# Performance work log

Measured on AMD Instinct MI355X. Metric: run time of the kernel, lower is better.

## Reference

```python
import jax, jax.numpy as jnp
import numpy as np

EMB_LEN = 1024
HEAD_SIZE = 64

def setup_inputs() -> dict:
    key = jax.random.key(0)
    k1, k2, k3, k4 = jax.random.split(key, 4)
    input_emb = jax.random.normal(k1, (8, 4096, EMB_LEN), dtype=jnp.float32)
    # nn.Linear weights are [out, in]; applied as x @ W.T
    Wq = jax.random.normal(k2, (HEAD_SIZE, EMB_LEN), dtype=jnp.float32) * (EMB_LEN ** -0.5)
    Wk = jax.random.normal(k3, (HEAD_SIZE, EMB_LEN), dtype=jnp.float32) * (EMB_LEN ** -0.5)
    Wv = jax.random.normal(k4, (HEAD_SIZE, EMB_LEN), dtype=jnp.float32) * (EMB_LEN ** -0.5)
    return {"input_emb": input_emb, "Wq": Wq, "Wk": Wk, "Wv": Wv}

def reference(input_emb, Wq, Wk, Wv):
    B, S, E = input_emb.shape
    scale = jnp.asarray(HEAD_SIZE, input_emb.dtype) ** -0.5
    q = jnp.einsum('bse,he->bsh', input_emb, Wq)  # [B,S,H]
    k = jnp.einsum('bse,he->bsh', input_emb, Wk)
    v = jnp.einsum('bse,he->bsh', input_emb, Wv)
    scores = jnp.einsum('bqh,bkh->bqk', q, k) * scale  # [B,S,S]
    causal = jnp.tril(jnp.ones((S, S), dtype=bool))
    scores = jnp.where(causal, scores, -jnp.inf)
    attn = jax.nn.softmax(scores, axis=-1)
    return jnp.einsum('bqk,bkh->bqh', attn, v)
```

## Files before the change

### kernel.cpp

```cpp
#include <hip/hip_runtime.h>
#include <hip/hip_bf16.h>

#define EMB 1024
#define HS 64
#define SEQ 4096

using bf16x8 = __attribute__((ext_vector_type(8))) __bf16;
using f32x4  = __attribute__((ext_vector_type(4))) float;

__device__ __forceinline__ ushort f2b(float f) {
    unsigned x = __float_as_uint(f);
    return (ushort)((x + 0x7fffu + ((x >> 16) & 1u)) >> 16);
}

__global__ void cvt_w(const float* __restrict__ wq, const float* __restrict__ wk,
                      const float* __restrict__ wv, ushort* __restrict__ wcat) {
    int i = blockIdx.x * 256 + threadIdx.x;
    const int n = HS * EMB;
    if (i >= 3 * n) return;
    float f;
    if (i < n)          f = wq[i];
    else if (i < 2 * n) f = wk[i - n];
    else                f = wv[i - 2 * n];
    wcat[i] = f2b(f);
}

__global__ __launch_bounds__(1024) void qkv_proj(
        const float* __restrict__ x, const ushort* __restrict__ wcat,
        ushort* __restrict__ qo, ushort* __restrict__ ko, ushort* __restrict__ vo) {
    __shared__ ushort Xs[64][72];
    __shared__ ushort Ws[192][72];
    const int t = threadIdx.x;
    const int lane = t & 63, wid = t >> 6;
    const int g = lane >> 4, c = lane & 15;
    const int strip = wid >> 2, colq = wid & 3;
    const int row0 = blockIdx.x * 64;

    f32x4 acc[3];
#pragma unroll
    for (int i = 0; i < 3; ++i) acc[i] = f32x4{0.f, 0.f, 0.f, 0.f};

    for (int kc = 0; kc < EMB; kc += 64) {
        __syncthreads();
        {
            int e = t * 4, r = e >> 6, cc = e & 63;
            float4 v = *reinterpret_cast<const float4*>(&x[(row0 + r) * EMB + kc + cc]);
            ushort4 u;
            u.x = f2b(v.x); u.y = f2b(v.y); u.z = f2b(v.z); u.w = f2b(v.w);
            *reinterpret_cast<ushort4*>(&Xs[r][cc]) = u;
        }
#pragma unroll
        for (int i = 0; i < 3; ++i) {
            int e = (i * 1024 + t) * 4, r = e >> 6, cc = e & 63;
            *reinterpret_cast<ushort4*>(&Ws[r][cc]) =
                *reinterpret_cast<const ushort4*>(&wcat[r * EMB + kc + cc]);
        }
        __syncthreads();
#pragma unroll
        for (int kk = 0; kk < 2; ++kk) {
            bf16x8 a = *reinterpret_cast<const bf16x8*>(&Xs[strip * 16 + c][kk * 32 + 8 * g]);
#pragma unroll
            for (int nt = 0; nt < 3; ++nt) {
                bf16x8 b = *reinterpret_cast<const bf16x8*>(
                    &Ws[(colq * 3 + nt) * 16 + c][kk * 32 + 8 * g]);
                acc[nt] = __builtin_amdgcn_mfma_f32_16x16x32_bf16(a, b, acc[nt], 0, 0, 0);
            }
        }
    }

    const float qs = 0.125f * 1.44269504f;
#pragma unroll
    for (int nt = 0; nt < 3; ++nt) {
        int col = (colq * 3 + nt) * 16 + c;
        int rowb = row0 + strip * 16 + 4 * g;
        if (col < 64) {
#pragma unroll
            for (int r = 0; r < 4; ++r)
                qo[(rowb + r) * 64 + col] = f2b(acc[nt][r] * qs);
        } else if (col < 128) {
#pragma unroll
            for (int r = 0; r < 4; ++r)
                ko[(rowb + r) * 64 + (col - 64)] = f2b(acc[nt][r]);
        } else {
            int b = rowb >> 12, s0 = rowb & 4095;
            ushort4 pv;
            pv.x = f2b(acc[nt][0]); pv.y = f2b(acc[nt][1]);
            pv.z = f2b(acc[nt][2]); pv.w = f2b(acc[nt][3]);
            *reinterpret_cast<ushort4*>(&vo[(b * 64 + (col - 128)) * SEQ + s0]) = pv;
        }
    }
}

__global__ __launch_bounds__(256) void attn(
        const ushort* __restrict__ q, const ushort* __restrict__ k,
        const ushort* __restrict__ vt, float* __restrict__ out) {
    __shared__ __align__(16) char smem[33280];

    const int t = threadIdx.x;
    const int lane = t & 63, w = t >> 6;
    const int g = lane >> 4, c = lane & 15;

    const int bid = blockIdx.x;
    const int batch = bid & 7;
    const int qt = 127 - (bid >> 3);
    const int q0 = qt * 32;
    const int nch = qt + 1;
    const int c0 = (w * nch) >> 2, c1 = ((w + 1) * nch) >> 2;

    const ushort* qb = q  + (size_t)batch * SEQ * 64;
    const ushort* kb = k  + (size_t)batch * SEQ * 64;
    const ushort* vb = vt + (size_t)batch * 64 * SEQ;

    bf16x8 qa[2][2];
#pragma unroll
    for (int ss = 0; ss < 2; ++ss)
#pragma unroll
        for (int kk = 0; kk < 2; ++kk)
            qa[ss][kk] = *reinterpret_cast<const bf16x8*>(
                &qb[(q0 + ss * 16 + c) * 64 + kk * 32 + 8 * g]);

    f32x4 accO[2][4];
#pragma unroll
    for (int ss = 0; ss < 2; ++ss)
#pragma unroll
        for (int nt = 0; nt < 4; ++nt) accO[ss][nt] = f32x4{0.f, 0.f, 0.f, 0.f};
    float lsum[2][4] = {{0.f, 0.f, 0.f, 0.f}, {0.f, 0.f, 0.f, 0.f}};

    char* const pslice = smem + w * 2048;
    const int pwr = (c >> 3) * 256 + g * 64 + (c & 7) * 2;

    auto loadkv = [&](bf16x8 (&kf)[2][2], bf16x8 (&vf)[4], int ch) {
        const int kv0 = ch * 32;
#pragma unroll
        for (int kt = 0; kt < 2; ++kt)
#pragma unroll
            for (int kk = 0; kk < 2; ++kk)
                kf[kt][kk] = *reinterpret_cast<const bf16x8*>(
                    &kb[(kv0 + kt * 16 + c) * 64 + kk * 32 + 8 * g]);
#pragma unroll
        for (int nt = 0; nt < 4; ++nt)
            vf[nt] = *reinterpret_cast<const bf16x8*>(
                &vb[(nt * 16 + c) * SEQ + kv0 + 8 * g]);
    };

    auto compute = [&](bf16x8 (&kf)[2][2], bf16x8 (&vf)[4], int ch) {
        f32x4 sA[2][2];
#pragma unroll
        for (int ss = 0; ss < 2; ++ss)
#pragma unroll
            for (int kt = 0; kt < 2; ++kt) sA[ss][kt] = f32x4{0.f, 0.f, 0.f, 0.f};
        __builtin_amdgcn_s_setprio(1);
#pragma unroll
        for (int kk = 0; kk < 2; ++kk)
#pragma unroll
            for (int kt = 0; kt < 2; ++kt) {
                sA[0][kt] = __builtin_amdgcn_mfma_f32_16x16x32_bf16(qa[0][kk], kf[kt][kk], sA[0][kt], 0, 0, 0);
                sA[1][kt] = __builtin_amdgcn_mfma_f32_16x16x32_bf16(qa[1][kk], kf[kt][kk], sA[1][kt], 0, 0, 0);
            }
        __builtin_amdgcn_s_setprio(0);

        if (ch == nch - 1) {
#pragma unroll
            for (int ss = 0; ss < 2; ++ss)
#pragma unroll
                for (int kt = 0; kt < 2; ++kt)
#pragma unroll
                    for (int r = 0; r < 4; ++r)
                        if (kt * 16 + c > ss * 16 + 4 * g + r) sA[ss][kt][r] = -INFINITY;
        }

#pragma unroll
        for (int ss = 0; ss < 2; ++ss)
#pragma unroll
            for (int kt = 0; kt < 2; ++kt)
#pragma unroll
                for (int r = 0; r < 4; ++r) {
                    float p = __builtin_amdgcn_exp2f(sA[ss][kt][r]);
                    lsum[ss][r] += p;
                    *(ushort*)(pslice + ss * 1024 + kt * 512 + r * 16 + pwr) = f2b(p);
                }

        bf16x8 pa0 = *reinterpret_cast<const bf16x8*>(pslice + lane * 16);
        bf16x8 pa1 = *reinterpret_cast<const bf16x8*>(pslice + 1024 + lane * 16);

        __builtin_amdgcn_s_setprio(1);
#pragma unroll
        for (int nt = 0; nt < 4; ++nt) {
            accO[0][nt] = __builtin_amdgcn_mfma_f32_16x16x32_bf16(pa0, vf[nt], accO[0][nt], 0, 0, 0);
            accO[1][nt] = __builtin_amdgcn_mfma_f32_16x16x32_bf16(pa1, vf[nt], accO[1][nt], 0, 0, 0);
        }
        __builtin_amdgcn_s_setprio(0);
    };

    bf16x8 kfA[2][2], vfA[4], kfB[2][2], vfB[4];
    int ch = c0;
    if (ch < c1) {
        loadkv(kfA, vfA, ch);
        while (true) {
            loadkv(kfB, vfB, (ch + 1 < c1) ? ch + 1 : ch);
            compute(kfA, vfA, ch);
            if (++ch >= c1) break;
            loadkv(kfA, vfA, (ch + 1 < c1) ? ch + 1 : ch);
            compute(kfB, vfB, ch);
            if (++ch >= c1) break;
        }
    }

#pragma unroll
    for (int off = 1; off < 16; off <<= 1)
#pragma unroll
        for (int ss = 0; ss < 2; ++ss)
#pragma unroll
            for (int r = 0; r < 4; ++r)
                lsum[ss][r] += __shfl_xor(lsum[ss][r], off, 64);

    __syncthreads();
#pragma unroll
    for (int ss = 0; ss < 2; ++ss)
#pragma unroll
        for (int nt = 0; nt < 4; ++nt)
#pragma unroll
            for (int r = 0; r < 4; ++r)
                *(float*)(smem + w * 8192 + (ss * 16 + 4 * g + r) * 256 + (nt * 16 + c) * 4) =
                    accO[ss][nt][r];
    if (c == 0) {
#pragma unroll
        for (int ss = 0; ss < 2; ++ss)
#pragma unroll
            for (int r = 0; r < 4; ++r)
                *(float*)(smem + 32768 + w * 128 + (ss * 16 + 4 * g + r) * 4) = lsum[ss][r];
    }
    __syncthreads();

    float* ob = out + (size_t)batch * SEQ * 64;
    const int col = t & 63, r0 = t >> 6;
#pragma unroll
    for (int rr = 0; rr < 8; ++rr) {
        int row = rr * 4 + r0;
        float s = 0.f, l = 0.f;
#pragma unroll
        for (int w4 = 0; w4 < 4; ++w4) {
            s += *(float*)(smem + w4 * 8192 + row * 256 + col * 4);
            l += *(float*)(smem + 32768 + w4 * 128 + row * 4);
        }
        ob[(q0 + row) * 64 + col] = s / l;
    }
}

extern "C" void kernel_launch(void* const* d_in, const int* in_sizes, int n_in,
                              void* d_out, int out_size, void* d_ws, size_t ws_size,
                              hipStream_t stream) {
    const float* x  = (const float*)d_in[0];
    const float* wq = (const float*)d_in[1];
    const float* wk = (const float*)d_in[2];
    const float* wv = (const float*)d_in[3];
    float* out = (float*)d_out;

    char* ws = (char*)d_ws;
    ushort* wcat = (ushort*)ws;
    ushort* qo   = (ushort*)(ws + 393216);
    ushort* ko   = (ushort*)(ws + 393216 + 4194304);
    ushort* vo   = (ushort*)(ws + 393216 + 2 * 4194304);

    hipLaunchKernelGGL(cvt_w, dim3(768), dim3(256), 0, stream, wq, wk, wv, wcat);
    hipLaunchKernelGGL(qkv_proj, dim3(512), dim3(1024), 0, stream, x, wcat, qo, ko, vo);
    hipLaunchKernelGGL(attn, dim3(1024), dim3(256), 0, stream, qo, ko, vo, out);
}
```

Measured before the change: 111.9 us.

## Split attention work per-wave with atomic reduction and register-shuffle P transpose

Each wave now owns an independent slice of KV chunks for a query tile, with the work split balanced so that groups of tiles get more waves as their causal length grows. Partial outputs and row sums are accumulated into global memory with atomicAdd, and a separate normalization kernel divides by the row sums. The S=K·Q^T operand order plus packed bf16 conversion and lane shuffles replace the LDS round trip for the probability matrix. This removes the shared-memory reduction, block-level syncs and double-buffered prefetch. In exchange it adds memsets, float atomics, an extra kernel launch and a non-deterministic summation order.

```diff
diff --git a/kernel.cpp b/kernel.cpp
--- a/kernel.cpp
+++ b/kernel.cpp
@@ -93,22 +93,30 @@
 
 __global__ __launch_bounds__(256) void attn(
         const ushort* __restrict__ q, const ushort* __restrict__ k,
-        const ushort* __restrict__ vt, float* __restrict__ out) {
-    __shared__ __align__(16) char smem[33280];
-
+        const ushort* __restrict__ vt, float* __restrict__ out, float* __restrict__ L) {
     const int t = threadIdx.x;
     const int lane = t & 63, w = t >> 6;
     const int g = lane >> 4, c = lane & 15;
 
-    const int bid = blockIdx.x;
-    const int batch = bid & 7;
-    const int qt = 127 - (bid >> 3);
+    const int wid = blockIdx.x * 4 + w;
+    const int batch = wid / 576;
+    const int rem = wid - batch * 576;
+    int G = 0;
+#pragma unroll
+    for (int gg = 1; gg < 8; ++gg) if (rem >= 8 * gg * (gg + 1)) G = gg;
+    const int per = G + 1;
+    const int off = rem - 8 * G * per;
+    const int j = off / per;
+    const int seg = off - j * per;
+    const int qt = 16 * G + j;
     const int q0 = qt * 32;
     const int nch = qt + 1;
-    const int c0 = (w * nch) >> 2, c1 = ((w + 1) * nch) >> 2;
-
-    const ushort* qb = q  + (size_t)batch * SEQ * 64;
-    const ushort* kb = k  + (size_t)batch * SEQ * 64;
+    const int Qd = nch / per, Rm = nch - Qd * per;
+    const int c0 = seg * Qd + (seg < Rm ? seg : Rm);
+    const int cnt = Qd + (seg < Rm ? 1 : 0);
+
+    const ushort* qb = q + (size_t)batch * SEQ * 64;
+    const ushort* kb = k + (size_t)batch * SEQ * 64;
     const ushort* vb = vt + (size_t)batch * 64 * SEQ;
 
     bf16x8 qa[2][2];
@@ -124,13 +132,15 @@
     for (int ss = 0; ss < 2; ++ss)
 #pragma unroll
         for (int nt = 0; nt < 4; ++nt) accO[ss][nt] = f32x4{0.f, 0.f, 0.f, 0.f};
-    float lsum[2][4] = {{0.f, 0.f, 0.f, 0.f}, {0.f, 0.f, 0.f, 0.f}};
-
-    char* const pslice = smem + w * 2048;
-    const int pwr = (c >> 3) * 256 + g * 64 + (c & 7) * 2;
-
-    auto loadkv = [&](bf16x8 (&kf)[2][2], bf16x8 (&vf)[4], int ch) {
+    float lsum[2] = {0.f, 0.f};
+
+    const int la = (2 * (g & 1)) * 16 + c;
+    const int lb = la + 16;
+    const bool glo = (g < 2);
+
+    for (int ch = c0; ch < c0 + cnt; ++ch) {
         const int kv0 = ch * 32;
+        bf16x8 kf[2][2], vf[4];
 #pragma unroll
         for (int kt = 0; kt < 2; ++kt)
 #pragma unroll
@@ -141,110 +151,94 @@
         for (int nt = 0; nt < 4; ++nt)
             vf[nt] = *reinterpret_cast<const bf16x8*>(
                 &vb[(nt * 16 + c) * SEQ + kv0 + 8 * g]);
-    };
-
-    auto compute = [&](bf16x8 (&kf)[2][2], bf16x8 (&vf)[4], int ch) {
+
         f32x4 sA[2][2];
 #pragma unroll
         for (int ss = 0; ss < 2; ++ss)
 #pragma unroll
             for (int kt = 0; kt < 2; ++kt) sA[ss][kt] = f32x4{0.f, 0.f, 0.f, 0.f};
-        __builtin_amdgcn_s_setprio(1);
 #pragma unroll
         for (int kk = 0; kk < 2; ++kk)
 #pragma unroll
             for (int kt = 0; kt < 2; ++kt) {
-                sA[0][kt] = __builtin_amdgcn_mfma_f32_16x16x32_bf16(qa[0][kk], kf[kt][kk], sA[0][kt], 0, 0, 0);
-                sA[1][kt] = __builtin_amdgcn_mfma_f32_16x16x32_bf16(qa[1][kk], kf[kt][kk], sA[1][kt], 0, 0, 0);
+                sA[0][kt] = __builtin_amdgcn_mfma_f32_16x16x32_bf16(kf[kt][kk], qa[0][kk], sA[0][kt], 0, 0, 0);
+                sA[1][kt] = __builtin_amdgcn_mfma_f32_16x16x32_bf16(kf[kt][kk], qa[1][kk], sA[1][kt], 0, 0, 0);
             }
-        __builtin_amdgcn_s_setprio(0);
-
-        if (ch == nch - 1) {
+
+        if (ch == qt) {
 #pragma unroll
             for (int ss = 0; ss < 2; ++ss)
 #pragma unroll
                 for (int kt = 0; kt < 2; ++kt)
 #pragma unroll
                     for (int r = 0; r < 4; ++r)
-                        if (kt * 16 + c > ss * 16 + 4 * g + r) sA[ss][kt][r] = -INFINITY;
-        }
-
+                        if (kv0 + kt * 16 + 4 * g + r > q0 + ss * 16 + c)
+                            sA[ss][kt][r] = -INFINITY;
+        }
+
+#pragma unroll
+        for (int ss = 0; ss < 2; ++ss) {
+            float p00 = __builtin_amdgcn_exp2f(sA[ss][0][0]);
+            float p01 = __builtin_amdgcn_exp2f(sA[ss][0][1]);
+            float p02 = __builtin_amdgcn_exp2f(sA[ss][0][2]);
+            float p03 = __builtin_amdgcn_exp2f(sA[ss][0][3]);
+            float p10 = __builtin_amdgcn_exp2f(sA[ss][1][0]);
+            float p11 = __builtin_amdgcn_exp2f(sA[ss][1][1]);
+            float p12 = __builtin_amdgcn_exp2f(sA[ss][1][2]);
+            float p13 = __builtin_amdgcn_exp2f(sA[ss][1][3]);
+            lsum[ss] += ((p00 + p01) + (p02 + p03)) + ((p10 + p11) + (p12 + p13));
+
+            uint dA0, dB0, dA1, dB1;
+            asm("v_cvt_pk_bf16_f32 %0, %1, %2" : "=v"(dA0) : "v"(p00), "v"(p01));
+            asm("v_cvt_pk_bf16_f32 %0, %1, %2" : "=v"(dB0) : "v"(p02), "v"(p03));
+            asm("v_cvt_pk_bf16_f32 %0, %1, %2" : "=v"(dA1) : "v"(p10), "v"(p11));
+            asm("v_cvt_pk_bf16_f32 %0, %1, %2" : "=v"(dB1) : "v"(p12), "v"(p13));
+
+            int s00 = __shfl((int)dA0, la, 64), s01 = __shfl((int)dB0, la, 64);
+            int s02 = __shfl((int)dA0, lb, 64), s03 = __shfl((int)dB0, lb, 64);
+            int s10 = __shfl((int)dA1, la, 64), s11 = __shfl((int)dB1, la, 64);
+            int s12 = __shfl((int)dA1, lb, 64), s13 = __shfl((int)dB1, lb, 64);
+            uint pw[4];
+            pw[0] = (uint)(glo ? s00 : s10);
+            pw[1] = (uint)(glo ? s01 : s11);
+            pw[2] = (uint)(glo ? s02 : s12);
+            pw[3] = (uint)(glo ? s03 : s13);
+            bf16x8 pa = *reinterpret_cast<bf16x8*>(pw);
+
+#pragma unroll
+            for (int nt = 0; nt < 4; ++nt)
+                accO[ss][nt] = __builtin_amdgcn_mfma_f32_16x16x32_bf16(pa, vf[nt], accO[ss][nt], 0, 0, 0);
+        }
+    }
+
+#pragma unroll
+    for (int ss = 0; ss < 2; ++ss) {
+        lsum[ss] += __shfl_xor(lsum[ss], 16, 64);
+        lsum[ss] += __shfl_xor(lsum[ss], 32, 64);
+    }
+    float* ob = out + (size_t)batch * SEQ * 64;
+#pragma unroll
+    for (int ss = 0; ss < 2; ++ss)
+#pragma unroll
+        for (int nt = 0; nt < 4; ++nt)
+#pragma unroll
+            for (int r = 0; r < 4; ++r)
+                atomicAdd(&ob[(size_t)(q0 + ss * 16 + 4 * g + r) * 64 + nt * 16 + c],
+                          accO[ss][nt][r]);
+    if (lane < 16) {
 #pragma unroll
         for (int ss = 0; ss < 2; ++ss)
-#pragma unroll
-            for (int kt = 0; kt < 2; ++kt)
-#pragma unroll
-                for (int r = 0; r < 4; ++r) {
-                    float p = __builtin_amdgcn_exp2f(sA[ss][kt][r]);
-                    lsum[ss][r] += p;
-                    *(ushort*)(pslice + ss * 1024 + kt * 512 + r * 16 + pwr) = f2b(p);
-                }
-
-        bf16x8 pa0 = *reinterpret_cast<const bf16x8*>(pslice + lane * 16);
-        bf16x8 pa1 = *reinterpret_cast<const bf16x8*>(pslice + 1024 + lane * 16);
-
-        __builtin_amdgcn_s_setprio(1);
-#pragma unroll
-        for (int nt = 0; nt < 4; ++nt) {
-            accO[0][nt] = __builtin_amdgcn_mfma_f32_16x16x32_bf16(pa0, vf[nt], accO[0][nt], 0, 0, 0);
-            accO[1][nt] = __builtin_amdgcn_mfma_f32_16x16x32_bf16(pa1, vf[nt], accO[1][nt], 0, 0, 0);
-        }
-        __builtin_amdgcn_s_setprio(0);
-    };
-
-    bf16x8 kfA[2][2], vfA[4], kfB[2][2], vfB[4];
-    int ch = c0;
-    if (ch < c1) {
-        loadkv(kfA, vfA, ch);
-        while (true) {
-            loadkv(kfB, vfB, (ch + 1 < c1) ? ch + 1 : ch);
-            compute(kfA, vfA, ch);
-            if (++ch >= c1) break;
-            loadkv(kfA, vfA, (ch + 1 < c1) ? ch + 1 : ch);
-            compute(kfB, vfB, ch);
-            if (++ch >= c1) break;
-        }
-    }
-
-#pragma unroll
-    for (int off = 1; off < 16; off <<= 1)
-#pragma unroll
-        for (int ss = 0; ss < 2; ++ss)
-#pragma unroll
-            for (int r = 0; r < 4; ++r)
-                lsum[ss][r] += __shfl_xor(lsum[ss][r], off, 64);
-
-    __syncthreads();
-#pragma unroll
-    for (int ss = 0; ss < 2; ++ss)
-#pragma unroll
-        for (int nt = 0; nt < 4; ++nt)
-#pragma unroll
-            for (int r = 0; r < 4; ++r)
-                *(float*)(smem + w * 8192 + (ss * 16 + 4 * g + r) * 256 + (nt * 16 + c) * 4) =
-                    accO[ss][nt][r];
-    if (c == 0) {
-#pragma unroll
-        for (int ss = 0; ss < 2; ++ss)
-#pragma unroll
-            for (int r = 0; r < 4; ++r)
-                *(float*)(smem + 32768 + w * 128 + (ss * 16 + 4 * g + r) * 4) = lsum[ss][r];
-    }
-    __syncthreads();
-
-    float* ob = out + (size_t)batch * SEQ * 64;
-    const int col = t & 63, r0 = t >> 6;
-#pragma unroll
-    for (int rr = 0; rr < 8; ++rr) {
-        int row = rr * 4 + r0;
-        float s = 0.f, l = 0.f;
-#pragma unroll
-        for (int w4 = 0; w4 < 4; ++w4) {
-            s += *(float*)(smem + w4 * 8192 + row * 256 + col * 4);
-            l += *(float*)(smem + 32768 + w4 * 128 + row * 4);
-        }
-        ob[(q0 + row) * 64 + col] = s / l;
-    }
+            atomicAdd(&L[batch * SEQ + q0 + ss * 16 + lane], lsum[ss]);
+    }
+}
+
+__global__ __launch_bounds__(256) void norm_out(float* __restrict__ out,
+                                                const float* __restrict__ L) {
+    int i = blockIdx.x * 256 + threadIdx.x;
+    float4 v = reinterpret_cast<float4*>(out)[i];
+    float inv = 1.0f / L[i >> 4];
+    v.x *= inv; v.y *= inv; v.z *= inv; v.w *= inv;
+    reinterpret_cast<float4*>(out)[i] = v;
 }
 
 extern "C" void kernel_launch(void* const* d_in, const int* in_sizes, int n_in,
@@ -261,8 +255,12 @@
     ushort* qo   = (ushort*)(ws + 393216);
     ushort* ko   = (ushort*)(ws + 393216 + 4194304);
     ushort* vo   = (ushort*)(ws + 393216 + 2 * 4194304);
-
+    float*  Lb   = (float*)(ws + 393216 + 3 * 4194304);
+
+    hipMemsetAsync(out, 0, (size_t)8 * SEQ * 64 * 4, stream);
+    hipMemsetAsync(Lb, 0, (size_t)8 * SEQ * 4, stream);
     hipLaunchKernelGGL(cvt_w, dim3(768), dim3(256), 0, stream, wq, wk, wv, wcat);
     hipLaunchKernelGGL(qkv_proj, dim3(512), dim3(1024), 0, stream, x, wcat, qo, ko, vo);
-    hipLaunchKernelGGL(attn, dim3(1024), dim3(256), 0, stream, qo, ko, vo, out);
-}
+    hipLaunchKernelGGL(attn, dim3(1152), dim3(256), 0, stream, qo, ko, vo, out, Lb);
+    hipLaunchKernelGGL(norm_out, dim3(2048), dim3(256), 0, stream, out, Lb);
+}
```

New measurement: 129.2 us. 1.15x slower.
